# Optimization experiments

Hardware: AMD Instinct MI355X
Metric: run time of the kernel (lower is better)

The kernel has to match this reference:

```python
import jax, jax.numpy as jnp
import numpy as np

B, C, T = 64, 128, 4096
KNOT = 4  # default knot=4 -> 6 spline knots
SIGMA = 0.2


def setup_inputs() -> dict:
    key = jax.random.key(0)
    k1, k2, k3 = jax.random.split(key, 3)
    x = jax.random.normal(k1, (B, C, T), dtype=jnp.float32)
    # yy ~ N(1.0, sigma) as in GenerateRandomCurves
    yy = 1.0 + SIGMA * jax.random.normal(k2, (B, KNOT + 2, C), dtype=jnp.float32)
    mask_rand = jax.random.uniform(k3, (B, 1, 1), dtype=jnp.float32)
    return {"x": x, "yy": yy, "mask_rand": mask_rand}


def _notaknot_matrix(n, h):
    # Moment (second-derivative) system for a not-a-knot cubic spline on a
    # uniform grid with spacing h (matches scipy.interpolate.CubicSpline default bc).
    A = np.zeros((n, n), dtype=np.float32)
    for i in range(1, n - 1):
        A[i, i - 1] = h / 6.0
        A[i, i] = 2.0 * h / 3.0
        A[i, i + 1] = h / 6.0
    # not-a-knot: third derivative continuous at x1 and x_{n-2}
    A[0, 0], A[0, 1], A[0, 2] = 1.0, -2.0, 1.0
    A[-1, -3], A[-1, -2], A[-1, -1] = 1.0, -2.0, 1.0
    return jnp.asarray(A)


def reference(x, yy, mask_rand):
    Bq, Cq, Tq = x.shape
    n = KNOT + 2
    h = (Tq - 1) / (KNOT + 1)  # uniform knot spacing; knots span [0, T-1]
    A = _notaknot_matrix(n, h)

    # Solve for spline moments M (second derivatives at knots), batched over (B, C).
    rhs_int = (yy[:, 2:, :] - 2.0 * yy[:, 1:-1, :] + yy[:, :-2, :]) / h  # (B, n-2, C)
    z = jnp.zeros((Bq, 1, Cq), yy.dtype)
    rhs = jnp.concatenate([z, rhs_int, z], axis=1)  # (B, n, C)
    M = jnp.linalg.solve(A, rhs)  # (B, n, C)

    # Evaluate the spline at t = 0..T-1 (vectorized over all batch/channel).
    tq = jnp.arange(Tq, dtype=x.dtype)
    idx = jnp.clip(jnp.floor(tq / h).astype(jnp.int32), 0, n - 2)  # (T,)
    xl = idx.astype(x.dtype) * h
    dxl = (tq - xl)[None, :, None]       # t - x_i
    dxr = (xl + h - tq)[None, :, None]   # x_{i+1} - t
    Mi, Mi1 = M[:, idx, :], M[:, idx + 1, :]      # (B, T, C)
    yi, yi1 = yy[:, idx, :], yy[:, idx + 1, :]    # (B, T, C)
    curve = ((Mi * dxr**3 + Mi1 * dxl**3) / (6.0 * h)
             + (yi / h - Mi * h / 6.0) * dxr
             + (yi1 / h - Mi1 * h / 6.0) * dxl)   # (B, T, C)

    # DistortTimesteps: cumulative sum, rescaled so the last step lands on T-1.
    tt = jnp.cumsum(curve, axis=1)
    tt = tt * (Tq - 1) / tt[:, -1:, :]  # (B, T, C)

    # Per-(batch, channel) linear interpolation back onto the regular grid.
    xp = tt.transpose(0, 2, 1).reshape(Bq * Cq, Tq)  # warped timestamps
    fp = x.reshape(Bq * Cq, Tq)                      # channel signals
    x_tw = jax.vmap(lambda a, b: jnp.interp(tq, a, b))(xp, fp)
    x_tw = x_tw.reshape(Bq, Cq, Tq)

    mask = mask_rand < 0.5  # (B,1,1): apply warp with probability p=0.5
    return jnp.where(mask, x_tw, x)
```

## Files before the change

### kernel.cpp

```cpp
#include <hip/hip_runtime.h>

#define BB 64
#define CC 128
#define TT 4096
#define NN 6
#define HH 819.0f

__device__ __forceinline__ int padi(int j) { return j + (j >> 5); }

__global__ __launch_bounds__(256) void timewarp_kernel(
    const float* __restrict__ x,
    const float* __restrict__ yy,
    const float* __restrict__ mask_rand,
    float* __restrict__ out)
{
    const int row = blockIdx.x;
    const int b   = row / CC;
    const int c   = row % CC;
    const int tid = threadIdx.x;

    const float* xrow = x + (size_t)row * TT;
    float* orow       = out + (size_t)row * TT;

    if (!(mask_rand[b] < 0.5f)) {
        const float4* xi = (const float4*)xrow;
        float4* oo = (float4*)orow;
        #pragma unroll
        for (int k = 0; k < 4; ++k) {
            int i = tid + 256 * k;
            oo[i] = xi[i];
        }
        return;
    }

    __shared__ float sh_fp[TT];
    __shared__ float sh_xp[TT + TT / 32];
    __shared__ float sh_part[256];
    __shared__ float sh_M[NN];
    __shared__ float sh_y[NN];

    {
        const float4* xi = (const float4*)xrow;
        float4* fp4 = (float4*)sh_fp;
        #pragma unroll
        for (int k = 0; k < 4; ++k) {
            int i = tid + 256 * k;
            fp4[i] = xi[i];
        }
    }

    if (tid == 0) {
        float y[NN];
        #pragma unroll
        for (int k = 0; k < NN; ++k)
            y[k] = yy[((size_t)b * NN + k) * CC + c];
        float Aug[NN][NN + 1];
        #pragma unroll
        for (int i = 0; i < NN; ++i)
            #pragma unroll
            for (int j = 0; j < NN + 1; ++j)
                Aug[i][j] = 0.0f;
        Aug[0][0] = 1.0f;  Aug[0][1] = -2.0f;  Aug[0][2] = 1.0f;
        Aug[5][3] = 1.0f;  Aug[5][4] = -2.0f;  Aug[5][5] = 1.0f;
        #pragma unroll
        for (int i = 1; i < NN - 1; ++i) {
            Aug[i][i - 1] = HH / 6.0f;
            Aug[i][i]     = 2.0f * HH / 3.0f;
            Aug[i][i + 1] = HH / 6.0f;
            Aug[i][NN]    = (y[i + 1] - 2.0f * y[i] + y[i - 1]) / HH;
        }
        #pragma unroll
        for (int k = 0; k < NN; ++k) {
            float inv = 1.0f / Aug[k][k];
            #pragma unroll
            for (int i = k + 1; i < NN; ++i) {
                float m = Aug[i][k] * inv;
                #pragma unroll
                for (int j = k; j < NN + 1; ++j)
                    Aug[i][j] -= m * Aug[k][j];
            }
        }
        float M[NN];
        #pragma unroll
        for (int i = NN - 1; i >= 0; --i) {
            float s = Aug[i][NN];
            #pragma unroll
            for (int j = i + 1; j < NN; ++j)
                s -= Aug[i][j] * M[j];
            M[i] = s / Aug[i][i];
        }
        #pragma unroll
        for (int k = 0; k < NN; ++k) { sh_M[k] = M[k]; sh_y[k] = y[k]; }
    }
    __syncthreads();

    const float inv6h = 1.0f / (6.0f * HH);
    const float hd6   = HH / 6.0f;
    const float invh  = 1.0f / HH;

    float loc[16];
    float running = 0.0f;
    const int t0 = tid * 16;
    #pragma unroll
    for (int k = 0; k < 16; ++k) {
        int t = t0 + k;
        int idx = t / 819;
        idx = idx > 4 ? 4 : idx;
        float xl  = (float)idx * HH;
        float ft  = (float)t;
        float dxl = ft - xl;
        float dxr = xl + HH - ft;
        float Mi  = sh_M[idx], Mi1 = sh_M[idx + 1];
        float yi  = sh_y[idx], yi1 = sh_y[idx + 1];
        float curve = (Mi * dxr * dxr * dxr + Mi1 * dxl * dxl * dxl) * inv6h
                    + (yi * invh - Mi * hd6) * dxr
                    + (yi1 * invh - Mi1 * hd6) * dxl;
        running += curve;
        loc[k] = running;
    }
    sh_part[tid] = running;
    __syncthreads();

    #pragma unroll
    for (int off = 1; off < 256; off <<= 1) {
        float v = (tid >= off) ? sh_part[tid - off] : 0.0f;
        __syncthreads();
        sh_part[tid] += v;
        __syncthreads();
    }
    float total = sh_part[255];
    float offs  = sh_part[tid] - running;
    float scale = 4095.0f / total;
    #pragma unroll
    for (int k = 0; k < 16; ++k)
        sh_xp[padi(t0 + k)] = (loc[k] + offs) * scale;
    __syncthreads();

    float res[16];
    int j;
    {
        float q0 = (float)t0;
        int lo = -1, hi = TT;
        while (hi - lo > 1) {
            int mid = (lo + hi) >> 1;
            if (sh_xp[padi(mid)] <= q0) lo = mid; else hi = mid;
        }
        j = lo;
    }
    #pragma unroll
    for (int k = 0; k < 16; ++k) {
        float q = (float)(t0 + k);
        while (j < TT - 1 && sh_xp[padi(j + 1)] <= q) ++j;
        float r;
        if (j < 0)            r = sh_fp[0];
        else if (j >= TT - 1) r = sh_fp[TT - 1];
        else {
            float x0 = sh_xp[padi(j)];
            float x1 = sh_xp[padi(j + 1)];
            float f0 = sh_fp[j];
            float f1 = sh_fp[j + 1];
            r = f0 + (q - x0) * (f1 - f0) / (x1 - x0);
        }
        res[k] = r;
    }

    float4* oo = (float4*)orow;
    #pragma unroll
    for (int k = 0; k < 4; ++k) {
        float4 v = make_float4(res[4*k], res[4*k+1], res[4*k+2], res[4*k+3]);
        oo[tid * 4 + k] = v;
    }
}

extern "C" void kernel_launch(void* const* d_in, const int* in_sizes, int n_in,
                              void* d_out, int out_size, void* d_ws, size_t ws_size,
                              hipStream_t stream) {
    const float* x    = (const float*)d_in[0];
    const float* yy   = (const float*)d_in[1];
    const float* mask = (const float*)d_in[2];
    float* out = (float*)d_out;
    timewarp_kernel<<<dim3(BB * CC), dim3(256), 0, stream>>>(x, yy, mask, out);
}
```

Baseline: 238.3 us.

## Scatter interpolation by source segment and use wave-shuffle scan

Replaces the per-query binary search plus forward walk with a scatter approach. Each thread owns 16 consecutive source segments of the monotone warped timestamps and writes the interpolated values for every integer query inside its segments into a shared result buffer. Each thread also solves the spline system redundantly in registers, reads x directly into registers, and replaces the 8-step shared-memory Hillis-Steele scan with wave-level shuffles plus a 4-entry cross-wave sum. This removes most barriers and the search latency. In exchange it adds load imbalance when segments stretch, and it relies on the warped timestamps being monotone.

```diff
diff --git a/kernel.cpp b/kernel.cpp
--- a/kernel.cpp
+++ b/kernel.cpp
@@ -33,24 +33,14 @@
         return;
     }
 
-    __shared__ float sh_fp[TT];
-    __shared__ float sh_xp[TT + TT / 32];
-    __shared__ float sh_part[256];
-    __shared__ float sh_M[NN];
-    __shared__ float sh_y[NN];
+    __shared__ float sh_res[TT + TT / 32];
+    __shared__ float sh_wsum[4];
+    __shared__ float sh_xf[256];
+    __shared__ float sh_ff[256];
 
+    float Mv[NN];
+    float y[NN];
     {
-        const float4* xi = (const float4*)xrow;
-        float4* fp4 = (float4*)sh_fp;
-        #pragma unroll
-        for (int k = 0; k < 4; ++k) {
-            int i = tid + 256 * k;
-            fp4[i] = xi[i];
-        }
-    }
-
-    if (tid == 0) {
-        float y[NN];
         #pragma unroll
         for (int k = 0; k < NN; ++k)
             y[k] = yy[((size_t)b * NN + k) * CC + c];
@@ -80,27 +70,33 @@
                     Aug[i][j] -= m * Aug[k][j];
             }
         }
-        float M[NN];
         #pragma unroll
         for (int i = NN - 1; i >= 0; --i) {
             float s = Aug[i][NN];
             #pragma unroll
             for (int j = i + 1; j < NN; ++j)
-                s -= Aug[i][j] * M[j];
-            M[i] = s / Aug[i][i];
+                s -= Aug[i][j] * Mv[j];
+            Mv[i] = s / Aug[i][i];
         }
+    }
+
+    const int t0 = tid * 16;
+    float fpv[17];
+    {
+        const float4* xi = (const float4*)(xrow + t0);
         #pragma unroll
-        for (int k = 0; k < NN; ++k) { sh_M[k] = M[k]; sh_y[k] = y[k]; }
+        for (int k = 0; k < 4; ++k) {
+            float4 v = xi[k];
+            fpv[4 * k + 0] = v.x; fpv[4 * k + 1] = v.y;
+            fpv[4 * k + 2] = v.z; fpv[4 * k + 3] = v.w;
+        }
     }
-    __syncthreads();
 
     const float inv6h = 1.0f / (6.0f * HH);
     const float hd6   = HH / 6.0f;
     const float invh  = 1.0f / HH;
-
     float loc[16];
     float running = 0.0f;
-    const int t0 = tid * 16;
     #pragma unroll
     for (int k = 0; k < 16; ++k) {
         int t = t0 + k;
@@ -110,65 +106,83 @@
         float ft  = (float)t;
         float dxl = ft - xl;
         float dxr = xl + HH - ft;
-        float Mi  = sh_M[idx], Mi1 = sh_M[idx + 1];
-        float yi  = sh_y[idx], yi1 = sh_y[idx + 1];
+        float Mi  = Mv[idx], Mi1 = Mv[idx + 1];
+        float yi  = y[idx],  yi1 = y[idx + 1];
         float curve = (Mi * dxr * dxr * dxr + Mi1 * dxl * dxl * dxl) * inv6h
                     + (yi * invh - Mi * hd6) * dxr
                     + (yi1 * invh - Mi1 * hd6) * dxl;
         running += curve;
         loc[k] = running;
     }
-    sh_part[tid] = running;
+
+    const int lane = tid & 63, wid = tid >> 6;
+    float ws = running;
+    #pragma unroll
+    for (int d = 1; d < 64; d <<= 1) {
+        float v = __shfl_up(ws, d, 64);
+        if (lane >= d) ws += v;
+    }
+    if (lane == 63) sh_wsum[wid] = ws;
     __syncthreads();
+    float wo = 0.0f, total = 0.0f;
+    #pragma unroll
+    for (int w = 0; w < 4; ++w) {
+        float s = sh_wsum[w];
+        total += s;
+        if (w < wid) wo += s;
+    }
+    const float offs  = wo + (ws - running);
+    const float scale = 4095.0f / total;
 
-    #pragma unroll
-    for (int off = 1; off < 256; off <<= 1) {
-        float v = (tid >= off) ? sh_part[tid - off] : 0.0f;
-        __syncthreads();
-        sh_part[tid] += v;
-        __syncthreads();
-    }
-    float total = sh_part[255];
-    float offs  = sh_part[tid] - running;
-    float scale = 4095.0f / total;
+    float xpv[17];
     #pragma unroll
     for (int k = 0; k < 16; ++k)
-        sh_xp[padi(t0 + k)] = (loc[k] + offs) * scale;
+        xpv[k] = (loc[k] + offs) * scale;
+
+    sh_xf[tid] = xpv[0];
+    sh_ff[tid] = fpv[0];
     __syncthreads();
+    xpv[16] = (tid < 255) ? sh_xf[tid + 1] : xpv[15];
+    fpv[16] = (tid < 255) ? sh_ff[tid + 1] : fpv[15];
 
-    float res[16];
-    int j;
-    {
-        float q0 = (float)t0;
-        int lo = -1, hi = TT;
-        while (hi - lo > 1) {
-            int mid = (lo + hi) >> 1;
-            if (sh_xp[padi(mid)] <= q0) lo = mid; else hi = mid;
-        }
-        j = lo;
+    if (tid == 0) {
+        int q1 = (int)ceilf(xpv[0]);
+        if (q1 > TT) q1 = TT;
+        for (int q = 0; q < q1; ++q) sh_res[padi(q)] = fpv[0];
     }
+    const int nseg = (tid < 255) ? 16 : 15;
     #pragma unroll
     for (int k = 0; k < 16; ++k) {
-        float q = (float)(t0 + k);
-        while (j < TT - 1 && sh_xp[padi(j + 1)] <= q) ++j;
-        float r;
-        if (j < 0)            r = sh_fp[0];
-        else if (j >= TT - 1) r = sh_fp[TT - 1];
-        else {
-            float x0 = sh_xp[padi(j)];
-            float x1 = sh_xp[padi(j + 1)];
-            float f0 = sh_fp[j];
-            float f1 = sh_fp[j + 1];
-            r = f0 + (q - x0) * (f1 - f0) / (x1 - x0);
+        if (k < nseg) {
+            float xa = xpv[k],  xb = xpv[k + 1];
+            float fa = fpv[k],  fb = fpv[k + 1];
+            int qlo = (int)ceilf(xa);  if (qlo < 0) qlo = 0;
+            int qhi = (int)ceilf(xb) - 1;  if (qhi > TT - 1) qhi = TT - 1;
+            float d = xb - xa;
+            float slope = (d > 0.0f) ? (fb - fa) / d : 0.0f;
+            for (int q = qlo; q <= qhi; ++q)
+                sh_res[padi(q)] = fa + ((float)q - xa) * slope;
         }
-        res[k] = r;
     }
+    if (tid == 255) {
+        int q0 = (int)ceilf(xpv[15]);
+        if (q0 < 0) q0 = 0;
+        for (int q = q0; q <= TT - 1; ++q) sh_res[padi(q)] = fpv[15];
+    }
+    __syncthreads();
 
     float4* oo = (float4*)orow;
     #pragma unroll
-    for (int k = 0; k < 4; ++k) {
-        float4 v = make_float4(res[4*k], res[4*k+1], res[4*k+2], res[4*k+3]);
-        oo[tid * 4 + k] = v;
+    for (int kk = 0; kk < 4; ++kk) {
+        int i4 = tid + 256 * kk;
+        int fb = 4 * i4;
+        int p  = padi(fb);
+        float4 v;
+        v.x = sh_res[p + 0];
+        v.y = sh_res[p + 1];
+        v.z = sh_res[p + 2];
+        v.w = sh_res[p + 3];
+        oo[i4] = v;
     }
 }
 
```

Result: no change. 237.3 us (-0.4%).
